# Kernel optimization log

Measured on AMD Instinct MI355X. Metric: run time of the kernel, lower is better.

Reference implementation:

```python
import jax, jax.numpy as jnp
import numpy as np

O_DIM = 16   # output_dim (number of output capsules)
H_POSE = 16  # h (pose/vector dim per capsule)
NUM_ROUTING = 3


def _squash(s):
    # norm over the pose dim (axis=2), matching torch _squash(dim=2)
    norm = jnp.linalg.norm(s, axis=2, keepdims=True)
    norm_sq = norm * norm
    return s / norm * (norm_sq / (1.0 + norm_sq))


def setup_inputs() -> dict:
    key = jax.random.key(0)
    k1, k2 = jax.random.split(key, 2)
    B, I, C, H, W = 8, 32, 8, 16, 16
    x = jax.random.normal(k1, (B, I, C, H, W), dtype=jnp.float32)
    # weight ~ N(0, 0.1): shape (I, C, O*h) (torch stores (I, C, O*h, 1, 1))
    weight = 0.1 * jax.random.normal(k2, (I, C, O_DIM * H_POSE), dtype=jnp.float32)
    # bias initialized to 0.1, shape (O, h, 1, 1)
    bias = jnp.full((O_DIM, H_POSE, 1, 1), 0.1, dtype=jnp.float32)
    return {"x": x, "weight": weight, "bias": bias}


def reference(x, weight, bias):
    B, I, C, H, W = x.shape
    O, h = O_DIM, H_POSE
    # votes[b,i,o*h,H,W] = sum_c x[b,i,c,H,W] * weight[i,c,o*h]
    votes = jnp.einsum('bichw,icm->bimhw', x, weight)
    votes = votes.reshape(B, I, O, h, H, W)

    logits = jnp.zeros((B, I, O, H, W), dtype=x.dtype)
    activation = None
    for i in range(NUM_ROUTING):
        route = jax.nn.softmax(logits, axis=2)  # softmax over output capsules O
        last = (i == NUM_ROUTING - 1)
        v = votes if last else jax.lax.stop_gradient(votes)
        # preactivate[b,o,h,H,W] = sum_i route * votes + bias
        preact = jnp.sum(route[:, :, :, None] * v, axis=1) + bias  # bias broadcasts (O,h,1,1)
        activation = _squash(preact)  # [B, O, h, H, W]
        if not last:
            # distances[b,i,o,H,W] = sum_h stop_grad(votes) * activation
            distances = jnp.sum(jax.lax.stop_gradient(votes) * activation[:, None], axis=3)
            logits = logits + distances
    return activation
```

## Files before the change

### kernel.cpp

```cpp
#include <hip/hip_runtime.h>
#include <math.h>


__device__ __forceinline__ float4 f4zero() { return make_float4(0.f, 0.f, 0.f, 0.f); }

__device__ __forceinline__ void fma4(float4& a, float s, const float4& q) {
    a.x = fmaf(s, q.x, a.x); a.y = fmaf(s, q.y, a.y);
    a.z = fmaf(s, q.z, a.z); a.w = fmaf(s, q.w, a.w);
}

__global__ __launch_bounds__(256, 2)
void caps_kernel(const float* __restrict__ x,
                 const float* __restrict__ wgt,
                 const float* __restrict__ bias,
                 float* __restrict__ out)
{
    __shared__ float s_route [4 * 512];
    __shared__ float s_logits[4 * 512];
    __shared__ float s_part  [16 * 256];
    __shared__ float s_act   [4 * 256];

    const int t   = threadIdx.x;
    const int w   = t >> 6;
    const int l   = t & 63;
    const int b   = blockIdx.x >> 6;
    const int hw0 = (blockIdx.x & 63) << 2;

    const float4 bias4 = ((const float4*)bias)[l];

    float4 v[8][4];
    {
        const float*  xb = x + (size_t)b * 65536 + hw0;
        const float4* w4 = (const float4*)wgt;
        #pragma unroll
        for (int ii = 0; ii < 8; ++ii) {
            const int i = __builtin_amdgcn_readfirstlane((w << 3) + ii);
            #pragma unroll
            for (int p = 0; p < 4; ++p) v[ii][p] = f4zero();
            #pragma unroll
            for (int c = 0; c < 8; ++c) {
                const float4 wv = w4[i * 512 + c * 64 + l];
                const float4 xv = *(const float4*)(xb + (i * 8 + c) * 256);
                fma4(v[ii][0], xv.x, wv);
                fma4(v[ii][1], xv.y, wv);
                fma4(v[ii][2], xv.z, wv);
                fma4(v[ii][3], xv.w, wv);
            }
        }
    }

    float4 actreg = f4zero();

    #pragma unroll
    for (int it = 0; it < 3; ++it) {
        float4 pre[4];
        if (it == 0) {
            #pragma unroll
            for (int p = 0; p < 4; ++p) {
                float4 s = v[0][p];
                #pragma unroll
                for (int ii = 1; ii < 8; ++ii) {
                    s.x += v[ii][p].x; s.y += v[ii][p].y;
                    s.z += v[ii][p].z; s.w += v[ii][p].w;
                }
                pre[p] = make_float4(s.x * 0.0625f, s.y * 0.0625f,
                                     s.z * 0.0625f, s.w * 0.0625f);
            }
        } else {
            const int base = w * 512 + (l >> 1) * 16 + (l & 1) * 8;
            const float4 la = *(const float4*)&s_logits[base];
            const float4 lb = *(const float4*)&s_logits[base + 4];
            float mx = fmaxf(fmaxf(fmaxf(la.x, la.y), fmaxf(la.z, la.w)),
                             fmaxf(fmaxf(lb.x, lb.y), fmaxf(lb.z, lb.w)));
            mx = fmaxf(mx, __shfl_xor(mx, 1));
            const float e0 = __expf(la.x - mx), e1 = __expf(la.y - mx);
            const float e2 = __expf(la.z - mx), e3 = __expf(la.w - mx);
            const float e4 = __expf(lb.x - mx), e5 = __expf(lb.y - mx);
            const float e6 = __expf(lb.z - mx), e7 = __expf(lb.w - mx);
            float sum = ((e0 + e1) + (e2 + e3)) + ((e4 + e5) + (e6 + e7));
            sum += __shfl_xor(sum, 1);
            const float inv = 1.f / sum;
            *(float4*)&s_route[base]     = make_float4(e0 * inv, e1 * inv, e2 * inv, e3 * inv);
            *(float4*)&s_route[base + 4] = make_float4(e4 * inv, e5 * inv, e6 * inv, e7 * inv);
            __syncthreads();

            #pragma unroll
            for (int p = 0; p < 4; ++p) pre[p] = f4zero();
            const int rb = w * 512 + (l >> 2);
            #pragma unroll
            for (int ii = 0; ii < 8; ++ii) {
                #pragma unroll
                for (int p = 0; p < 4; ++p) {
                    const float r = s_route[rb + p * 128 + ii * 16];
                    fma4(pre[p], r, v[ii][p]);
                }
            }
        }

        #pragma unroll
        for (int p = 0; p < 4; ++p)
            *(float4*)&s_part[(w * 4 + p) * 256 + 4 * l] = pre[p];
        __syncthreads();

        float4 acc = bias4;
        #pragma unroll
        for (int wp = 0; wp < 4; ++wp) {
            const float4 q = *(const float4*)&s_part[(wp * 4 + w) * 256 + 4 * l];
            acc.x += q.x; acc.y += q.y; acc.z += q.z; acc.w += q.w;
        }
        float sq = acc.x * acc.x + acc.y * acc.y + acc.z * acc.z + acc.w * acc.w;
        sq += __shfl_xor(sq, 1);
        sq += __shfl_xor(sq, 2);
        const float f = sqrtf(sq) / (1.f + sq);
        actreg = make_float4(acc.x * f, acc.y * f, acc.z * f, acc.w * f);

        if (it < 2) {
            *(float4*)&s_act[w * 256 + 4 * l] = actreg;
            __syncthreads();

            float dacc[8];
            #pragma unroll
            for (int ii = 0; ii < 8; ++ii) dacc[ii] = 0.f;
            #pragma unroll
            for (int p = 0; p < 4; ++p) {
                const float4 a = *(const float4*)&s_act[p * 256 + 4 * l];
                #pragma unroll
                for (int ii = 0; ii < 8; ++ii) {
                    float d = v[ii][p].x * a.x + v[ii][p].y * a.y
                            + v[ii][p].z * a.z + v[ii][p].w * a.w;
                    d += __shfl_xor(d, 1);
                    d += __shfl_xor(d, 2);
                    dacc[ii] = ((l & 3) == p) ? d : dacc[ii];
                }
            }
            const int lb2 = w * 512 + (l & 3) * 128 + (l >> 2);
            if (it == 0) {
                #pragma unroll
                for (int ii = 0; ii < 8; ++ii) s_logits[lb2 + ii * 16] = dacc[ii];
            } else {
                #pragma unroll
                for (int ii = 0; ii < 8; ++ii) s_logits[lb2 + ii * 16] += dacc[ii];
            }
            __syncthreads();
        }
    }

    *(float4*)&s_act[w * 256 + 4 * l] = actreg;
    __syncthreads();
    float4 o4;
    o4.x = s_act[t];
    o4.y = s_act[256 + t];
    o4.z = s_act[512 + t];
    o4.w = s_act[768 + t];
    *(float4*)(out + (size_t)b * 65536 + (size_t)t * 256 + hw0) = o4;
}

extern "C" void kernel_launch(void* const* d_in, const int* in_sizes, int n_in,
                              void* d_out, int out_size, void* d_ws, size_t ws_size,
                              hipStream_t stream) {
    const float* x    = (const float*)d_in[0];
    const float* wgt  = (const float*)d_in[1];
    const float* bias = (const float*)d_in[2];
    float* out = (float*)d_out;
    caps_kernel<<<dim3(512), dim3(256), 0, stream>>>(x, wgt, bias, out);
}
```

Before: 71.77 us.

## Split input capsules across eight waves per block and relayout routing buffers

Doubles the block to 512 threads so each wave holds votes for 4 input capsules instead of 8. This halves per-thread register use and lets more waves hide latency. The logits and route shared-memory layout becomes row-major per (p,i,o), with a 4-lane softmax. The partial-sum reduction now reads 8 wave slices instead of 4. The cost is more shared-memory traffic in the cross-wave reduction, and barriers now span twice as many waves.

```diff
diff --git a/kernel.cpp b/kernel.cpp
--- a/kernel.cpp
+++ b/kernel.cpp
@@ -9,7 +9,11 @@
     a.z = fmaf(s, q.z, a.z); a.w = fmaf(s, q.w, a.w);
 }
 
-__global__ __launch_bounds__(256, 2)
+__device__ __forceinline__ void add4(float4& a, const float4& q) {
+    a.x += q.x; a.y += q.y; a.z += q.z; a.w += q.w;
+}
+
+__global__ __launch_bounds__(512, 4)
 void caps_kernel(const float* __restrict__ x,
                  const float* __restrict__ wgt,
                  const float* __restrict__ bias,
@@ -17,7 +21,7 @@
 {
     __shared__ float s_route [4 * 512];
     __shared__ float s_logits[4 * 512];
-    __shared__ float s_part  [16 * 256];
+    __shared__ float s_part  [8 * 4 * 256];
     __shared__ float s_act   [4 * 256];
 
     const int t   = threadIdx.x;
@@ -28,13 +32,13 @@
 
     const float4 bias4 = ((const float4*)bias)[l];
 
-    float4 v[8][4];
+    float4 v[4][4];
     {
         const float*  xb = x + (size_t)b * 65536 + hw0;
         const float4* w4 = (const float4*)wgt;
         #pragma unroll
-        for (int ii = 0; ii < 8; ++ii) {
-            const int i = __builtin_amdgcn_readfirstlane((w << 3) + ii);
+        for (int ii = 0; ii < 4; ++ii) {
+            const int i = __builtin_amdgcn_readfirstlane((w << 2) + ii);
             #pragma unroll
             for (int p = 0; p < 4; ++p) v[ii][p] = f4zero();
             #pragma unroll
@@ -50,6 +54,8 @@
     }
 
     float4 actreg = f4zero();
+    const int o  = l >> 2;
+    const int pw = w & 3;
 
     #pragma unroll
     for (int it = 0; it < 3; ++it) {
@@ -59,39 +65,34 @@
             for (int p = 0; p < 4; ++p) {
                 float4 s = v[0][p];
                 #pragma unroll
-                for (int ii = 1; ii < 8; ++ii) {
-                    s.x += v[ii][p].x; s.y += v[ii][p].y;
-                    s.z += v[ii][p].z; s.w += v[ii][p].w;
-                }
+                for (int ii = 1; ii < 4; ++ii) add4(s, v[ii][p]);
                 pre[p] = make_float4(s.x * 0.0625f, s.y * 0.0625f,
                                      s.z * 0.0625f, s.w * 0.0625f);
             }
         } else {
-            const int base = w * 512 + (l >> 1) * 16 + (l & 1) * 8;
-            const float4 la = *(const float4*)&s_logits[base];
-            const float4 lb = *(const float4*)&s_logits[base + 4];
-            float mx = fmaxf(fmaxf(fmaxf(la.x, la.y), fmaxf(la.z, la.w)),
-                             fmaxf(fmaxf(lb.x, lb.y), fmaxf(lb.z, lb.w)));
+            const int row  = (w << 4) + (l >> 2);
+            const int base = row * 16 + ((l & 3) << 2);
+            const float4 lg = *(const float4*)&s_logits[base];
+            float mx = fmaxf(fmaxf(lg.x, lg.y), fmaxf(lg.z, lg.w));
             mx = fmaxf(mx, __shfl_xor(mx, 1));
-            const float e0 = __expf(la.x - mx), e1 = __expf(la.y - mx);
-            const float e2 = __expf(la.z - mx), e3 = __expf(la.w - mx);
-            const float e4 = __expf(lb.x - mx), e5 = __expf(lb.y - mx);
-            const float e6 = __expf(lb.z - mx), e7 = __expf(lb.w - mx);
-            float sum = ((e0 + e1) + (e2 + e3)) + ((e4 + e5) + (e6 + e7));
-            sum += __shfl_xor(sum, 1);
-            const float inv = 1.f / sum;
-            *(float4*)&s_route[base]     = make_float4(e0 * inv, e1 * inv, e2 * inv, e3 * inv);
-            *(float4*)&s_route[base + 4] = make_float4(e4 * inv, e5 * inv, e6 * inv, e7 * inv);
+            mx = fmaxf(mx, __shfl_xor(mx, 2));
+            const float e0 = __expf(lg.x - mx), e1 = __expf(lg.y - mx);
+            const float e2 = __expf(lg.z - mx), e3 = __expf(lg.w - mx);
+            float sm = (e0 + e1) + (e2 + e3);
+            sm += __shfl_xor(sm, 1);
+            sm += __shfl_xor(sm, 2);
+            const float inv = 1.f / sm;
+            *(float4*)&s_route[base] = make_float4(e0 * inv, e1 * inv, e2 * inv, e3 * inv);
             __syncthreads();
 
             #pragma unroll
             for (int p = 0; p < 4; ++p) pre[p] = f4zero();
-            const int rb = w * 512 + (l >> 2);
             #pragma unroll
-            for (int ii = 0; ii < 8; ++ii) {
+            for (int ii = 0; ii < 4; ++ii) {
+                const int i = (w << 2) + ii;
                 #pragma unroll
                 for (int p = 0; p < 4; ++p) {
-                    const float r = s_route[rb + p * 128 + ii * 16];
+                    const float r = s_route[p * 512 + i * 16 + o];
                     fma4(pre[p], r, v[ii][p]);
                 }
             }
@@ -104,10 +105,8 @@
 
         float4 acc = bias4;
         #pragma unroll
-        for (int wp = 0; wp < 4; ++wp) {
-            const float4 q = *(const float4*)&s_part[(wp * 4 + w) * 256 + 4 * l];
-            acc.x += q.x; acc.y += q.y; acc.z += q.z; acc.w += q.w;
-        }
+        for (int wp = 0; wp < 8; ++wp)
+            add4(acc, *(const float4*)&s_part[(wp * 4 + pw) * 256 + 4 * l]);
         float sq = acc.x * acc.x + acc.y * acc.y + acc.z * acc.z + acc.w * acc.w;
         sq += __shfl_xor(sq, 1);
         sq += __shfl_xor(sq, 2);
@@ -115,17 +114,15 @@
         actreg = make_float4(acc.x * f, acc.y * f, acc.z * f, acc.w * f);
 
         if (it < 2) {
-            *(float4*)&s_act[w * 256 + 4 * l] = actreg;
+            if (w < 4) *(float4*)&s_act[w * 256 + 4 * l] = actreg;
             __syncthreads();
 
-            float dacc[8];
-            #pragma unroll
-            for (int ii = 0; ii < 8; ++ii) dacc[ii] = 0.f;
+            float dacc[4] = {0.f, 0.f, 0.f, 0.f};
             #pragma unroll
             for (int p = 0; p < 4; ++p) {
                 const float4 a = *(const float4*)&s_act[p * 256 + 4 * l];
                 #pragma unroll
-                for (int ii = 0; ii < 8; ++ii) {
+                for (int ii = 0; ii < 4; ++ii) {
                     float d = v[ii][p].x * a.x + v[ii][p].y * a.y
                             + v[ii][p].z * a.z + v[ii][p].w * a.w;
                     d += __shfl_xor(d, 1);
@@ -133,26 +130,28 @@
                     dacc[ii] = ((l & 3) == p) ? d : dacc[ii];
                 }
             }
-            const int lb2 = w * 512 + (l & 3) * 128 + (l >> 2);
+            const int lb = (l & 3) * 512 + (w << 2) * 16 + o;
             if (it == 0) {
                 #pragma unroll
-                for (int ii = 0; ii < 8; ++ii) s_logits[lb2 + ii * 16] = dacc[ii];
+                for (int ii = 0; ii < 4; ++ii) s_logits[lb + ii * 16] = dacc[ii];
             } else {
                 #pragma unroll
-                for (int ii = 0; ii < 8; ++ii) s_logits[lb2 + ii * 16] += dacc[ii];
+                for (int ii = 0; ii < 4; ++ii) s_logits[lb + ii * 16] += dacc[ii];
             }
             __syncthreads();
         }
     }
 
-    *(float4*)&s_act[w * 256 + 4 * l] = actreg;
+    if (w < 4) *(float4*)&s_act[w * 256 + 4 * l] = actreg;
     __syncthreads();
-    float4 o4;
-    o4.x = s_act[t];
-    o4.y = s_act[256 + t];
-    o4.z = s_act[512 + t];
-    o4.w = s_act[768 + t];
-    *(float4*)(out + (size_t)b * 65536 + (size_t)t * 256 + hw0) = o4;
+    if (t < 256) {
+        float4 o4;
+        o4.x = s_act[t];
+        o4.y = s_act[256 + t];
+        o4.z = s_act[512 + t];
+        o4.w = s_act[768 + t];
+        *(float4*)(out + (size_t)b * 65536 + (size_t)t * 256 + hw0) = o4;
+    }
 }
 
 extern "C" void kernel_launch(void* const* d_in, const int* in_sizes, int n_in,
@@ -162,5 +161,5 @@
     const float* wgt  = (const float*)d_in[1];
     const float* bias = (const float*)d_in[2];
     float* out = (float*)d_out;
-    caps_kernel<<<dim3(512), dim3(256), 0, stream>>>(x, wgt, bias, out);
+    caps_kernel<<<dim3(512), dim3(512), 0, stream>>>(x, wgt, bias, out);
 }
```

Result: no change. 72.26 us (+0.7%).
